# Kernel optimization log

Measured on AMD Instinct MI355X. Metric: run time of the kernel, lower is better.

The kernel has to match this reference:

```python
import jax, jax.numpy as jnp
import numpy as np

SDIM, VDIM, HID, DEPTH = 128, 3, 64, 4
N, E = 50000, 800000
CUTOFF = 5.0


def setup_inputs() -> dict:
    key = jax.random.key(0)
    ks = jax.random.split(key, 16)
    s = jax.random.normal(ks[0], (N, SDIM), jnp.float32)
    v = jax.random.normal(ks[1], (N, 3, VDIM), jnp.float32)
    edge_index = jax.random.randint(ks[2], (2, E), 0, N, dtype=jnp.int32).astype(jnp.int64)
    d = jax.random.uniform(ks[3], (E,), jnp.float32) * CUTOFF
    r = jax.random.normal(ks[4], (E, 3), jnp.float32)
    r = r / jnp.linalg.norm(r, axis=-1, keepdims=True)
    batch = jnp.zeros((N,), jnp.int64)

    def w(k, shape):
        return jax.random.normal(k, shape, jnp.float32) / jnp.sqrt(jnp.float32(shape[-2]))

    return {
        's': s, 'v': v, 'edge_index': edge_index, 'd': d, 'r': r, 'batch': batch,
        'We1': w(ks[5], (DEPTH, 2 * SDIM + 1, HID)), 'be1': jnp.zeros((DEPTH, HID), jnp.float32),
        'We2': w(ks[6], (DEPTH, HID, HID)), 'be2': jnp.zeros((DEPTH, HID), jnp.float32),
        'Wn1': w(ks[7], (DEPTH, SDIM + HID, HID)), 'bn1': jnp.zeros((DEPTH, HID), jnp.float32),
        'Wn2': w(ks[8], (DEPTH, HID, SDIM)), 'bn2': jnp.zeros((DEPTH, SDIM), jnp.float32),
        'Wv': w(ks[9], (DEPTH, HID, 2 * VDIM)), 'bv': jnp.zeros((DEPTH, 2 * VDIM), jnp.float32),
    }


def _egcl(s, v, src, dst, d, r, C, deg, We1, be1, We2, be2, Wn1, bn1, Wn2, bn2, Wv, bv):
    n = s.shape[0]
    # edge message MLP on gathered endpoint features + distance
    x = jnp.concatenate([s[dst], s[src], d[:, None]], axis=-1)   # [E, 2*SDIM+1]
    h = jax.nn.silu(x @ We1 + be1)
    h = jax.nn.silu(h @ We2 + be2)
    h = h * C[:, None]                                            # cutoff envelope
    # scalar update
    agg_s = jax.ops.segment_sum(h, dst, num_segments=n)           # [N, HID]
    u = jax.nn.silu(jnp.concatenate([s, agg_s], axis=-1) @ Wn1 + bn1)
    s = s + (u @ Wn2 + bn2)
    # equivariant vector update: gated neighbor vectors + gated edge directions
    gates = h @ Wv + bv                                           # [E, 2*VDIM]
    g1, g2 = gates[:, :VDIM], gates[:, VDIM:]
    mv = v[src] * g1[:, None, :] + r[:, :, None] * g2[:, None, :] # [E, 3, VDIM]
    agg_v = jax.ops.segment_sum(mv, dst, num_segments=n) / deg[:, None, None]  # mean aggr
    v = v + agg_v
    return s, v


def reference(s, v, edge_index, d, r, batch, We1, be1, We2, be2, Wn1, bn1, Wn2, bn2, Wv, bv):
    src, dst = edge_index[0], edge_index[1]
    C = 0.5 * (jnp.cos(jnp.pi * d / CUTOFF) + 1.0) * (d < CUTOFF).astype(d.dtype)
    deg = jax.ops.segment_sum(jnp.ones_like(d), dst, num_segments=s.shape[0])
    deg = jnp.maximum(deg, 1.0)
    for i in range(DEPTH):
        s, v = _egcl(s, v, src, dst, d, r, C, deg,
                     We1[i], be1[i], We2[i], be2[i],
                     Wn1[i], bn1[i], Wn2[i], bn2[i], Wv[i], bv[i])
    return (s, v)
```

## Files before the change

kernel.cpp:

```cpp
#include <hip/hip_runtime.h>
#include <math.h>

#define SDIM 128
#define HID 64
#define DEPTH 4
#define CUTOFF_F 5.0f
#define CHUNK 4096

typedef __attribute__((ext_vector_type(8))) short bf16x8;
typedef __attribute__((ext_vector_type(4))) float f32x4;
typedef float4 __attribute__((aligned(4))) float4_u;

__device__ __forceinline__ float silu_f(float x) {
    float e = __expf(-x);
    return x * __builtin_amdgcn_rcpf(1.0f + e);
}

__device__ __forceinline__ unsigned short f2bf(float x) {
    __bf16 b = (__bf16)x;
    return __builtin_bit_cast(unsigned short, b);
}
__device__ __forceinline__ unsigned int f2bf2(float a, float b) {
    return (unsigned int)f2bf(a) | ((unsigned int)f2bf(b) << 16);
}
__device__ __forceinline__ float bf2f(unsigned short u) {
    return __uint_as_float(((unsigned int)u) << 16);
}

struct f8 { float v[8]; };
__device__ __forceinline__ f8 load8(const float* p) {
    f8 r;
    float4 a = *(const float4*)p;
    float4 b = *(const float4*)(p + 4);
    r.v[0]=a.x; r.v[1]=a.y; r.v[2]=a.z; r.v[3]=a.w;
    r.v[4]=b.x; r.v[5]=b.y; r.v[6]=b.z; r.v[7]=b.w;
    return r;
}
__device__ __forceinline__ bf16x8 pack8(const float* h) {
    bf16x8 o;
#pragma unroll
    for (int j = 0; j < 8; ++j) o[j] = (short)f2bf(h[j]);
    return o;
}
__device__ __forceinline__ void unpack8(bf16x8 b, float* o) {
#pragma unroll
    for (int j = 0; j < 8; ++j)
        o[j] = __uint_as_float(((unsigned int)(unsigned short)b[j]) << 16);
}

__global__ void detect_idx_kernel(const void* ei, int N, int* flag) {
    int lane = threadIdx.x;
    const long long* p64 = (const long long*)ei;
    long long v = p64[lane];
    bool ok = (v >= 0 && v < (long long)N);
    unsigned long long m = __ballot(ok);
    if (lane == 0) *flag = (m == ~0ull) ? 1 : 0;
}

__global__ void decode_idx_kernel(const void* ei, int E, int N, const int* flag,
                                  int* __restrict__ srcw, int* __restrict__ dstw,
                                  int* __restrict__ deg_i) {
    int i = blockIdx.x * blockDim.x + threadIdx.x;
    if (i >= 2 * E) return;
    int v;
    if (*flag) v = (int)((const long long*)ei)[i];
    else       v = ((const int*)ei)[i];
    v = min(max(v, 0), N - 1);
    if (i < E) {
        srcw[i] = v;
    } else {
        dstw[i - E] = v;
        atomicAdd(&deg_i[v], 1);
    }
}

__global__ __launch_bounds__(256) void scan1_kernel(const int* __restrict__ deg_i,
                                                    int* __restrict__ part, int N) {
    __shared__ int wsum[4];
    int b = blockIdx.x, t = threadIdx.x;
    int base = b * CHUNK;
    int sum = 0;
    for (int i = t; i < CHUNK; i += 256) {
        int idx = base + i;
        sum += (idx < N) ? deg_i[idx] : 0;
    }
#pragma unroll
    for (int off = 32; off; off >>= 1) sum += __shfl_down(sum, off, 64);
    if ((t & 63) == 0) wsum[t >> 6] = sum;
    __syncthreads();
    if (t == 0) part[b] = wsum[0] + wsum[1] + wsum[2] + wsum[3];
}

__global__ void scan2_kernel(int* __restrict__ part, int* __restrict__ row_start,
                             int B1, int N) {
    int t = threadIdx.x;
    int v = (t < B1) ? part[t] : 0;
    int incl = v;
#pragma unroll
    for (int off = 1; off < 64; off <<= 1) {
        int x = __shfl_up(incl, off, 64);
        if (t >= off) incl += x;
    }
    if (t < B1) part[t] = incl - v;
    if (t == 63) row_start[N] = incl;
}

__global__ __launch_bounds__(256) void scan3_kernel(const int* __restrict__ deg_i,
                                                    const int* __restrict__ part,
                                                    int* __restrict__ row_start, int N) {
    __shared__ int wsum[4];
    __shared__ int carry_s;
    int b = blockIdx.x, t = threadIdx.x;
    int lane = t & 63, w = t >> 6;
    if (t == 0) carry_s = part[b];
    __syncthreads();
    int base0 = b * CHUNK;
    for (int base = base0; base < base0 + CHUNK; base += 256) {
        int i = base + t;
        int v = (i < N) ? deg_i[i] : 0;
        int incl = v;
#pragma unroll
        for (int off = 1; off < 64; off <<= 1) {
            int x = __shfl_up(incl, off, 64);
            if (lane >= off) incl += x;
        }
        if (lane == 63) wsum[w] = incl;
        __syncthreads();
        int wpre = 0;
#pragma unroll
        for (int k = 0; k < 4; ++k) if (k < w) wpre += wsum[k];
        int total = wsum[0] + wsum[1] + wsum[2] + wsum[3];
        int carry = carry_s;
        if (i < N) row_start[i] = carry + wpre + incl - v;
        __syncthreads();
        if (t == 0) carry_s = carry + total;
        __syncthreads();
    }
}

__global__ void scatter_kernel(const int* __restrict__ srcw, const int* __restrict__ dstw,
                               const float* __restrict__ dvec, const float* __restrict__ rvec,
                               const int* __restrict__ row_start, int* __restrict__ cursor,
                               float* __restrict__ rec, int E) {
    int e = blockIdx.x * blockDim.x + threadIdx.x;
    if (e >= E) return;
    int dd = dstw[e];
    int ofs = atomicAdd(&cursor[dd], 1);
    int pos = row_start[dd] + ofs;
    float dv = dvec[e];
    float c = 0.5f * (cosf(3.14159265358979323846f * dv * (1.0f / CUTOFF_F)) + 1.0f);
    c = (dv < CUTOFF_F) ? c : 0.0f;
    float4 r0 = make_float4(__int_as_float(srcw[e]), __int_as_float(dd), dv, c);
    float4 r1 = make_float4(rvec[(size_t)e * 3 + 0], rvec[(size_t)e * 3 + 1],
                            rvec[(size_t)e * 3 + 2], 0.0f);
    *(float4*)(rec + (size_t)pos * 8)     = r0;
    *(float4*)(rec + (size_t)pos * 8 + 4) = r1;
}

__global__ __launch_bounds__(256) void wprep_kernel(
    const float* __restrict__ We1, const float* __restrict__ We2,
    const float* __restrict__ Wv,  const float* __restrict__ Wn1,
    const float* __restrict__ Wn2,
    unsigned short* __restrict__ We1t, unsigned short* __restrict__ We2t,
    unsigned short* __restrict__ Wvt,  unsigned short* __restrict__ Wn1t,
    unsigned short* __restrict__ Wn2t) {
    int l = blockIdx.x, t = threadIdx.x;
    const float* W2 = We2 + (size_t)l * HID * HID;
    unsigned short* T2 = We2t + (size_t)l * HID * HID;
    for (int idx = t; idx < HID * HID; idx += 256) {
        int n = idx >> 6, k = idx & 63;
        T2[n * 64 + k] = f2bf(W2[k * HID + n]);
    }
    const float* Wvl = Wv + (size_t)l * HID * 6;
    unsigned short* Tv = Wvt + (size_t)l * 16 * 64;
    for (int idx = t; idx < 16 * 64; idx += 256) {
        int n = idx >> 6, k = idx & 63;
        Tv[idx] = (n < 6) ? f2bf(Wvl[k * 6 + n]) : (unsigned short)0;
    }
    const float* W1 = We1 + (size_t)l * 257 * 64;
    unsigned short* T1 = We1t + (size_t)l * 128 * 128;
    for (int idx = t; idx < 128 * 128; idx += 256) {
        int n = idx >> 7, k = idx & 127;
        float w = (n < 64) ? W1[(size_t)k * 64 + n] : W1[(size_t)(k + 128) * 64 + (n - 64)];
        T1[n * 128 + k] = f2bf(w);
    }
    const float* Wn1l = Wn1 + (size_t)l * 192 * 64;
    unsigned short* Tn1 = Wn1t + (size_t)l * 64 * 192;
    for (int idx = t; idx < 64 * 192; idx += 256) {
        int n = idx / 192, k = idx - n * 192;
        Tn1[idx] = f2bf(Wn1l[(size_t)k * 64 + n]);
    }
    const float* Wn2l = Wn2 + (size_t)l * 64 * 128;
    unsigned short* Tn2 = Wn2t + (size_t)l * 128 * 64;
    for (int idx = t; idx < 128 * 64; idx += 256) {
        int n = idx >> 6, k = idx & 63;
        Tn2[idx] = f2bf(Wn2l[(size_t)k * 128 + n]);
    }
}

__global__ __launch_bounds__(256) void node_pre_kernel(
    const float* __restrict__ s, const unsigned short* __restrict__ We1t,
    const float* __restrict__ be1,
    unsigned short* __restrict__ Pa, unsigned short* __restrict__ Pb, int N)
{
    __shared__ unsigned short sa[64 * 136];
    int t = threadIdx.x;
    int n0 = blockIdx.x * 64;
    for (int idx = t; idx < 64 * 32; idx += 256) {
        int rn = idx >> 5, c4 = (idx & 31) << 2;
        int n = n0 + rn;
        float4 val = make_float4(0.f, 0.f, 0.f, 0.f);
        if (n < N) val = *(const float4*)(s + (size_t)n * SDIM + c4);
        *(uint2*)(sa + rn * 136 + c4) = make_uint2(f2bf2(val.x, val.y), f2bf2(val.z, val.w));
    }
    __syncthreads();
    int lane = t & 63, w = t >> 6;
    int lm = lane & 15, lq = lane >> 4;
    int m0 = w * 16, rm = m0 + lm;

    bf16x8 af[4];
#pragma unroll
    for (int kc = 0; kc < 4; ++kc)
        af[kc] = *(const bf16x8*)(sa + rm * 136 + kc * 32 + lq * 8);

#pragma unroll
    for (int ct = 0; ct < 8; ++ct) {
        int col = ct * 16 + lm;
        f32x4 acc = {0.f, 0.f, 0.f, 0.f};
#pragma unroll
        for (int kc = 0; kc < 4; ++kc) {
            bf16x8 b = *(const bf16x8*)(We1t + (size_t)col * 128 + kc * 32 + lq * 8);
            acc = __builtin_amdgcn_mfma_f32_16x16x32_bf16(af[kc], b, acc, 0, 0, 0);
        }
        float bias = (ct < 4) ? be1[col] : 0.0f;
#pragma unroll
        for (int g = 0; g < 4; ++g) {
            int n = n0 + m0 + lq * 4 + g;
            if (n < N) {
                if (ct < 4) Pa[(size_t)n * HID + col]        = f2bf(acc[g] + bias);
                else        Pb[(size_t)n * HID + (col - 64)] = f2bf(acc[g]);
            }
        }
    }
}

__global__ __launch_bounds__(256) void edge_kernel(
    const float* __restrict__ rec,
    const unsigned short* __restrict__ Pa, const unsigned short* __restrict__ Pb,
    const float* __restrict__ wd,
    const unsigned short* __restrict__ We2t, const float* __restrict__ be2,
    const unsigned short* __restrict__ Wvt, const float* __restrict__ bv,
    const float* __restrict__ v,
    float* __restrict__ agg_s, float* __restrict__ agg_v, int E)
{
    __shared__ unsigned short hb[64 * 72];
    __shared__ float gl[64 * 8];
    __shared__ float vb[64 * 12];
    __shared__ float recb[64 * 8];
    int t = threadIdx.x;
    int e0 = blockIdx.x * 64;

    if (e0 + 64 <= E) {
        float2 rv = *(const float2*)(rec + (size_t)e0 * 8 + 2 * t);
        *(float2*)(recb + 2 * t) = rv;
    } else {
        int r = t >> 2, c = (t & 3) * 2;
        int e = e0 + r;
        int ec = (e < E) ? e : (E - 1);
        float a  = rec[(size_t)ec * 8 + c];
        float b2 = rec[(size_t)ec * 8 + c + 1];
        if (e >= E && c == 2) b2 = 0.0f;
        recb[2 * t]     = a;
        recb[2 * t + 1] = b2;
    }
    __syncthreads();

    int lane = t & 63;
    int w    = t >> 6;
    int lm = lane & 15, lq = lane >> 4;
    int m0 = w * 16;
    int rm = m0 + lm;
    int ka = lq * 8;
    int kb = 32 + lq * 8;

    {
        int r = t >> 2, p = t & 3;
        const float* vr = v + (size_t)__float_as_int(recb[r * 8]) * 9;
        if (p < 2) {
            float4_u a = *(const float4_u*)(vr + p * 4);
            vb[r * 12 + p * 4 + 0] = a.x;
            vb[r * 12 + p * 4 + 1] = a.y;
            vb[r * 12 + p * 4 + 2] = a.z;
            vb[r * 12 + p * 4 + 3] = a.w;
        } else if (p == 2) {
            vb[r * 12 + 8] = vr[8];
        }
    }
    bf16x8 wv0 = *(const bf16x8*)(Wvt + (size_t)lm * 64 + ka);
    bf16x8 wv1 = *(const bf16x8*)(Wvt + (size_t)lm * 64 + kb);

    bf16x8 afr0, afr1;
    {
        int srcr = __float_as_int(recb[rm * 8 + 0]);
        int dstr = __float_as_int(recb[rm * 8 + 1]);
        float dv = recb[rm * 8 + 2];
        const unsigned short* pa = Pa + (size_t)dstr * HID;
        const unsigned short* pb = Pb + (size_t)srcr * HID;
        bf16x8 ba0 = *(const bf16x8*)(pa + ka);
        bf16x8 bb0 = *(const bf16x8*)(pb + ka);
        bf16x8 ba1 = *(const bf16x8*)(pa + kb);
        bf16x8 bb1 = *(const bf16x8*)(pb + kb);
        f8 xw = load8(wd + ka), yw = load8(wd + kb);
        float fa[8], fb[8], h1[8];
        unpack8(ba0, fa); unpack8(bb0, fb);
#pragma unroll
        for (int j = 0; j < 8; ++j) h1[j] = silu_f(fa[j] + fb[j] + dv * xw.v[j]);
        afr0 = pack8(h1);
        unpack8(ba1, fa); unpack8(bb1, fb);
#pragma unroll
        for (int j = 0; j < 8; ++j) h1[j] = silu_f(fa[j] + fb[j] + dv * yw.v[j]);
        afr1 = pack8(h1);
    }

    float cc[4];
#pragma unroll
    for (int g = 0; g < 4; ++g) cc[g] = recb[(m0 + lq * 4 + g) * 8 + 3];
#pragma unroll
    for (int t4 = 0; t4 < 4; ++t4) {
        int col = t4 * 16 + lm;
        bf16x8 b0 = *(const bf16x8*)(We2t + (size_t)col * 64 + ka);
        bf16x8 b1 = *(const bf16x8*)(We2t + (size_t)col * 64 + kb);
        f32x4 a = {0.f, 0.f, 0.f, 0.f};
        a = __builtin_amdgcn_mfma_f32_16x16x32_bf16(afr0, b0, a, 0, 0, 0);
        a = __builtin_amdgcn_mfma_f32_16x16x32_bf16(afr1, b1, a, 0, 0, 0);
        float bias = be2[col];
#pragma unroll
        for (int g = 0; g < 4; ++g) {
            int er = m0 + lq * 4 + g;
            hb[er * 72 + col] = f2bf(silu_f(a[g] + bias) * cc[g]);
        }
    }
    __syncthreads();

    {
        bf16x8 hb0 = *(const bf16x8*)(hb + rm * 72 + ka);
        bf16x8 hb1 = *(const bf16x8*)(hb + rm * 72 + kb);
        f32x4 ga = {0.f, 0.f, 0.f, 0.f};
        ga = __builtin_amdgcn_mfma_f32_16x16x32_bf16(wv0, hb0, ga, 0, 0, 0);
        ga = __builtin_amdgcn_mfma_f32_16x16x32_bf16(wv1, hb1, ga, 0, 0, 0);
        int er2 = m0 + lm;
        if (lq == 0) {
            float4_u bb = *(const float4_u*)bv;
            *(float4*)(gl + er2 * 8) =
                make_float4(ga[0] + bb.x, ga[1] + bb.y, ga[2] + bb.z, ga[3] + bb.w);
        } else if (lq == 1) {
            gl[er2 * 8 + 4] = ga[0] + bv[4];
            gl[er2 * 8 + 5] = ga[1] + bv[5];
        }
    }

    {
        int c = t & 63, seg = t >> 6;
        int r0s = seg * 16;
        float acc = 0.f;
        int cur = __float_as_int(recb[r0s * 8 + 1]);
#pragma unroll 4
        for (int r = r0s; r < r0s + 16; ++r) {
            int dr = __float_as_int(recb[r * 8 + 1]);
            if (dr != cur) {
                atomicAdd(&agg_s[(size_t)cur * HID + c], acc);
                acc = 0.f; cur = dr;
            }
            acc += bf2f(hb[r * 72 + c]);
        }
        atomicAdd(&agg_s[(size_t)cur * HID + c], acc);
    }
    __syncthreads();

    if (t < 144) {
        int seg = t / 9;
        int c = t - seg * 9;
        int i = c / 3, j = c - i * 3;
        int r0v = seg * 4;
        float acc = 0.f;
        int cur = __float_as_int(recb[r0v * 8 + 1]);
#pragma unroll
        for (int r = 0; r < 4; ++r) {
            int rr = r0v + r;
            int dr = __float_as_int(recb[rr * 8 + 1]);
            if (dr != cur) {
                atomicAdd(&agg_v[(size_t)cur * 9 + c], acc);
                acc = 0.f; cur = dr;
            }
            if (e0 + rr < E) {
                acc += vb[rr * 12 + c] * gl[rr * 8 + j]
                     + recb[rr * 8 + 4 + i] * gl[rr * 8 + 3 + j];
            }
        }
        atomicAdd(&agg_v[(size_t)cur * 9 + c], acc);
    }
}

__global__ __launch_bounds__(256) void node_fused_kernel(
    float* __restrict__ s, float* __restrict__ vout,
    float* __restrict__ agg_s, float* __restrict__ agg_v,
    const int* __restrict__ row_start,
    const unsigned short* __restrict__ Wn1t, const float* __restrict__ bn1,
    const unsigned short* __restrict__ Wn2t, const float* __restrict__ bn2,
    const unsigned short* __restrict__ We1tn, const float* __restrict__ be1n,
    unsigned short* __restrict__ Pa, unsigned short* __restrict__ Pb,
    int N, int do_pre)
{
    __shared__ unsigned short xa[64 * 200];
    __shared__ unsigned short ub[64 * 72];
    int t = threadIdx.x;
    int n0 = blockIdx.x * 64;
    for (int idx = t; idx < 64 * 32; idx += 256) {
        int rn = idx >> 5, c4 = (idx & 31) << 2;
        int n = n0 + rn;
        float4 val = make_float4(0.f, 0.f, 0.f, 0.f);
        if (n < N) val = *(const float4*)(s + (size_t)n * SDIM + c4);
        *(uint2*)(xa + rn * 200 + c4) = make_uint2(f2bf2(val.x, val.y), f2bf2(val.z, val.w));
    }
    for (int idx = t; idx < 64 * 16; idx += 256) {
        int rn = idx >> 4, c4 = (idx & 15) << 2;
        int n = n0 + rn;
        float4 val = make_float4(0.f, 0.f, 0.f, 0.f);
        if (n < N) {
            float* ap = agg_s + (size_t)n * HID + c4;
            val = *(const float4*)ap;
            *(float4*)ap = make_float4(0.f, 0.f, 0.f, 0.f);
        }
        *(uint2*)(xa + rn * 200 + 128 + c4) = make_uint2(f2bf2(val.x, val.y), f2bf2(val.z, val.w));
    }
    __syncthreads();

    int lane = t & 63, w = t >> 6;
    int lm = lane & 15, lq = lane >> 4;
    int m0 = w * 16, rm = m0 + lm;

    bf16x8 af[6];
#pragma unroll
    for (int kc = 0; kc < 6; ++kc)
        af[kc] = *(const bf16x8*)(xa + rm * 200 + kc * 32 + lq * 8);

#pragma unroll
    for (int ct = 0; ct < 4; ++ct) {
        int col = ct * 16 + lm;
        f32x4 acc = {0.f, 0.f, 0.f, 0.f};
#pragma unroll
        for (int kc = 0; kc < 6; ++kc) {
            bf16x8 b = *(const bf16x8*)(Wn1t + (size_t)col * 192 + kc * 32 + lq * 8);
            acc = __builtin_amdgcn_mfma_f32_16x16x32_bf16(af[kc], b, acc, 0, 0, 0);
        }
        float bias = bn1[col];
#pragma unroll
        for (int g = 0; g < 4; ++g) {
            int er = m0 + lq * 4 + g;
            ub[er * 72 + col] = f2bf(silu_f(acc[g] + bias));
        }
    }
    __syncthreads();

    unsigned short* sa = xa;
    bf16x8 uf[2];
#pragma unroll
    for (int kc = 0; kc < 2; ++kc)
        uf[kc] = *(const bf16x8*)(ub + rm * 72 + kc * 32 + lq * 8);

#pragma unroll
    for (int ct = 0; ct < 8; ++ct) {
        int col = ct * 16 + lm;
        f32x4 acc = {0.f, 0.f, 0.f, 0.f};
#pragma unroll
        for (int kc = 0; kc < 2; ++kc) {
            bf16x8 b = *(const bf16x8*)(Wn2t + (size_t)col * 64 + kc * 32 + lq * 8);
            acc = __builtin_amdgcn_mfma_f32_16x16x32_bf16(uf[kc], b, acc, 0, 0, 0);
        }
        float bias = bn2[col];
#pragma unroll
        for (int g = 0; g < 4; ++g) {
            int er = m0 + lq * 4 + g;
            int n = n0 + er;
            if (n < N) {
                float* sp = s + (size_t)n * SDIM + col;
                float sv = *sp + acc[g] + bias;
                *sp = sv;
                sa[er * 136 + col] = f2bf(sv);
            } else {
                sa[er * 136 + col] = 0;
            }
        }
    }
    __syncthreads();

    if (do_pre) {
        bf16x8 pf[4];
#pragma unroll
        for (int kc = 0; kc < 4; ++kc)
            pf[kc] = *(const bf16x8*)(sa + rm * 136 + kc * 32 + lq * 8);

#pragma unroll
        for (int ct = 0; ct < 8; ++ct) {
            int col = ct * 16 + lm;
            f32x4 acc = {0.f, 0.f, 0.f, 0.f};
#pragma unroll
            for (int kc = 0; kc < 4; ++kc) {
                bf16x8 b = *(const bf16x8*)(We1tn + (size_t)col * 128 + kc * 32 + lq * 8);
                acc = __builtin_amdgcn_mfma_f32_16x16x32_bf16(pf[kc], b, acc, 0, 0, 0);
            }
            float bias = (ct < 4) ? be1n[col] : 0.0f;
#pragma unroll
            for (int g = 0; g < 4; ++g) {
                int n = n0 + m0 + lq * 4 + g;
                if (n < N) {
                    if (ct < 4) Pa[(size_t)n * HID + col]        = f2bf(acc[g] + bias);
                    else        Pb[(size_t)n * HID + (col - 64)] = f2bf(acc[g]);
                }
            }
        }
    }

    for (int idx = t; idx < 64 * 9; idx += 256) {
        int rn = idx / 9, c = idx - rn * 9;
        int n2 = n0 + rn;
        if (n2 < N) {
            float av = agg_v[(size_t)n2 * 9 + c];
            agg_v[(size_t)n2 * 9 + c] = 0.f;
            float dg = fmaxf((float)(row_start[n2 + 1] - row_start[n2]), 1.0f);
            vout[(size_t)n2 * 9 + c] += av / dg;
        }
    }
}

extern "C" void kernel_launch(void* const* d_in, const int* in_sizes, int n_in,
                              void* d_out, int out_size, void* d_ws, size_t ws_size,
                              hipStream_t stream)
{
    const float* s_in  = (const float*)d_in[0];
    const float* v_in  = (const float*)d_in[1];
    const void*  ei    = d_in[2];
    const float* d_vec = (const float*)d_in[3];
    const float* r_vec = (const float*)d_in[4];
    const float* We1 = (const float*)d_in[6];
    const float* be1 = (const float*)d_in[7];
    const float* We2 = (const float*)d_in[8];
    const float* be2 = (const float*)d_in[9];
    const float* Wn1 = (const float*)d_in[10];
    const float* bn1 = (const float*)d_in[11];
    const float* Wn2 = (const float*)d_in[12];
    const float* bn2 = (const float*)d_in[13];
    const float* Wv  = (const float*)d_in[14];
    const float* bv  = (const float*)d_in[15];

    int N = in_sizes[0] / SDIM;
    int E = in_sizes[3];

    float* out_s = (float*)d_out;
    float* out_v = out_s + (size_t)N * SDIM;

    char* wp = (char*)d_ws;
    auto alloc = [&wp](size_t bytes) -> char* {
        char* p = wp;
        wp += (bytes + 31) & ~(size_t)31;
        return p;
    };
    float* rec       = (float*)alloc((size_t)E * 8 * 4);
    unsigned short* Pa = (unsigned short*)alloc((size_t)N * HID * 2);
    unsigned short* Pb = (unsigned short*)alloc((size_t)N * HID * 2);
    float* agg_s     = (float*)alloc((size_t)N * HID * 4);
    float* agg_v     = (float*)alloc((size_t)N * 9 * 4);
    int*   deg_i     = (int*)alloc((size_t)N * 4);
    int*   cursor    = (int*)alloc((size_t)N * 4);
    int*   row_start = (int*)alloc((size_t)(N + 1) * 4);
    int*   part      = (int*)alloc(64 * 4);
    int*   flag      = (int*)alloc(16);
    int*   srcw      = (int*)alloc((size_t)E * 4);
    int*   dstw      = (int*)alloc((size_t)E * 4);
    unsigned short* We2t = (unsigned short*)alloc((size_t)DEPTH * HID * HID * 2);
    unsigned short* Wvt  = (unsigned short*)alloc((size_t)DEPTH * 16 * 64 * 2);
    unsigned short* We1t = (unsigned short*)alloc((size_t)DEPTH * 128 * 128 * 2);
    unsigned short* Wn1t = (unsigned short*)alloc((size_t)DEPTH * 64 * 192 * 2);
    unsigned short* Wn2t = (unsigned short*)alloc((size_t)DEPTH * 128 * 64 * 2);

    hipMemcpyAsync(out_s, s_in, (size_t)N * SDIM * sizeof(float),
                   hipMemcpyDeviceToDevice, stream);
    hipMemcpyAsync(out_v, v_in, (size_t)N * 9 * sizeof(float),
                   hipMemcpyDeviceToDevice, stream);

    detect_idx_kernel<<<1, 64, 0, stream>>>(ei, N, flag);
    hipMemsetAsync(deg_i, 0, (size_t)N * 2 * sizeof(int), stream);
    hipMemsetAsync(agg_s, 0, (size_t)N * (HID + 9) * sizeof(float), stream);
    decode_idx_kernel<<<(2 * E + 255) / 256, 256, 0, stream>>>(ei, E, N, flag,
                                                               srcw, dstw, deg_i);
    int B1 = (N + CHUNK - 1) / CHUNK;
    scan1_kernel<<<B1, 256, 0, stream>>>(deg_i, part, N);
    scan2_kernel<<<1, 64, 0, stream>>>(part, row_start, B1, N);
    scan3_kernel<<<B1, 256, 0, stream>>>(deg_i, part, row_start, N);
    scatter_kernel<<<(E + 255) / 256, 256, 0, stream>>>(srcw, dstw, d_vec, r_vec,
                                                        row_start, cursor, rec, E);
    wprep_kernel<<<DEPTH, 256, 0, stream>>>(We1, We2, Wv, Wn1, Wn2,
                                            We1t, We2t, Wvt, Wn1t, Wn2t);

    int nb_n = (N + 63) / 64;
    int nb_e = (E + 63) / 64;
    node_pre_kernel<<<nb_n, 256, 0, stream>>>(out_s, We1t, be1, Pa, Pb, N);
    for (int l = 0; l < DEPTH; ++l) {
        int ln = (l + 1 < DEPTH) ? (l + 1) : 0;
        const float* We1_l = We1 + (size_t)l * 257 * 64;
        const float* be2_l = be2 + (size_t)l * 64;
        const float* bn1_l = bn1 + (size_t)l * 64;
        const float* bn2_l = bn2 + (size_t)l * 128;
        const float* bv_l  = bv  + (size_t)l * 6;
        const float* be1_n = be1 + (size_t)ln * 64;
        const unsigned short* We2t_l = We2t + (size_t)l * HID * HID;
        const unsigned short* Wvt_l  = Wvt  + (size_t)l * 16 * 64;
        const unsigned short* Wn1t_l = Wn1t + (size_t)l * 64 * 192;
        const unsigned short* Wn2t_l = Wn2t + (size_t)l * 128 * 64;
        const unsigned short* We1t_n = We1t + (size_t)ln * 128 * 128;

        edge_kernel<<<nb_e, 256, 0, stream>>>(rec, Pa, Pb,
                                              We1_l + 256 * 64,
                                              We2t_l, be2_l, Wvt_l, bv_l,
                                              out_v, agg_s, agg_v, E);
        node_fused_kernel<<<nb_n, 256, 0, stream>>>(out_s, out_v, agg_s, agg_v,
                                                    row_start,
                                                    Wn1t_l, bn1_l, Wn2t_l, bn2_l,
                                                    We1t_n, be1_n, Pa, Pb,
                                                    N, (l + 1 < DEPTH) ? 1 : 0);
    }
}
```

Baseline: 823.1 us.

## Make edge and node kernels wave-local, replacing block barriers with wave barriers

Each wave now owns its 16-row slice of shared memory in the edge, node-pre and node-update kernels, so block-wide __syncthreads are replaced by wave barriers. In the edge kernel the per-edge record is loaded straight into registers with one float4 per row, and the endpoint gathers are issued right away instead of first staging the whole record in LDS. Only dst, C and r are kept in shared memory for the scatter phase. This removes block synchronization stalls and a staging round-trip, at the cost of some redundant record loads across lanes and reliance on wave barriers for correct LDS ordering.

```diff
diff --git a/kernel.cpp b/kernel.cpp
--- a/kernel.cpp
+++ b/kernel.cpp
@@ -203,25 +203,26 @@
     const float* __restrict__ be1,
     unsigned short* __restrict__ Pa, unsigned short* __restrict__ Pb, int N)
 {
-    __shared__ unsigned short sa[64 * 136];
+    __shared__ unsigned short sa[4][16 * 136];
     int t = threadIdx.x;
+    int lane = t & 63, w = t >> 6;
     int n0 = blockIdx.x * 64;
-    for (int idx = t; idx < 64 * 32; idx += 256) {
-        int rn = idx >> 5, c4 = (idx & 31) << 2;
-        int n = n0 + rn;
+    int m0 = w * 16;
+    unsigned short* sw = sa[w];
+    for (int idx = lane; idx < 512; idx += 64) {
+        int rl = idx >> 5, c4 = (idx & 31) << 2;
+        int n = n0 + m0 + rl;
         float4 val = make_float4(0.f, 0.f, 0.f, 0.f);
         if (n < N) val = *(const float4*)(s + (size_t)n * SDIM + c4);
-        *(uint2*)(sa + rn * 136 + c4) = make_uint2(f2bf2(val.x, val.y), f2bf2(val.z, val.w));
-    }
-    __syncthreads();
-    int lane = t & 63, w = t >> 6;
+        *(uint2*)(sw + rl * 136 + c4) = make_uint2(f2bf2(val.x, val.y), f2bf2(val.z, val.w));
+    }
+    __builtin_amdgcn_wave_barrier();
     int lm = lane & 15, lq = lane >> 4;
-    int m0 = w * 16, rm = m0 + lm;
 
     bf16x8 af[4];
 #pragma unroll
     for (int kc = 0; kc < 4; ++kc)
-        af[kc] = *(const bf16x8*)(sa + rm * 136 + kc * 32 + lq * 8);
+        af[kc] = *(const bf16x8*)(sw + lm * 136 + kc * 32 + lq * 8);
 
 #pragma unroll
     for (int ct = 0; ct < 8; ++ct) {
@@ -254,46 +255,46 @@
     float* __restrict__ agg_s, float* __restrict__ agg_v, int E)
 {
     __shared__ unsigned short hb[64 * 72];
-    __shared__ float gl[64 * 8];
-    __shared__ float vb[64 * 12];
-    __shared__ float recb[64 * 8];
+    __shared__ float  gl[64 * 8];
+    __shared__ float  vb[64 * 12];
+    __shared__ int    m_dst[64];
+    __shared__ float  m_C[64];
+    __shared__ float4 m_r4[64];
     int t = threadIdx.x;
     int e0 = blockIdx.x * 64;
-
-    if (e0 + 64 <= E) {
-        float2 rv = *(const float2*)(rec + (size_t)e0 * 8 + 2 * t);
-        *(float2*)(recb + 2 * t) = rv;
-    } else {
-        int r = t >> 2, c = (t & 3) * 2;
-        int e = e0 + r;
-        int ec = (e < E) ? e : (E - 1);
-        float a  = rec[(size_t)ec * 8 + c];
-        float b2 = rec[(size_t)ec * 8 + c + 1];
-        if (e >= E && c == 2) b2 = 0.0f;
-        recb[2 * t]     = a;
-        recb[2 * t + 1] = b2;
-    }
-    __syncthreads();
-
-    int lane = t & 63;
-    int w    = t >> 6;
+    int lane = t & 63, w = t >> 6;
     int lm = lane & 15, lq = lane >> 4;
-    int m0 = w * 16;
-    int rm = m0 + lm;
-    int ka = lq * 8;
-    int kb = 32 + lq * 8;
-
+    int m0 = w * 16, rm = m0 + lm;
+    int ka = lq * 8, kb = 32 + lq * 8;
+
+    int e  = e0 + rm;
+    int ec = min(e, E - 1);
+    float4 r0 = *(const float4*)(rec + (size_t)ec * 8);
+    int srcr = __float_as_int(r0.x);
+    int dstr = __float_as_int(r0.y);
+    float dv = r0.z;
+    float Cr = (e < E) ? r0.w : 0.0f;
+
+    const unsigned short* pa = Pa + (size_t)dstr * HID;
+    const unsigned short* pb = Pb + (size_t)srcr * HID;
+    bf16x8 ba0 = *(const bf16x8*)(pa + ka);
+    bf16x8 bb0 = *(const bf16x8*)(pb + ka);
+    bf16x8 ba1 = *(const bf16x8*)(pa + kb);
+    bf16x8 bb1 = *(const bf16x8*)(pb + kb);
+    f8 xw = load8(wd + ka), yw = load8(wd + kb);
+
+    if (lq == 0) {
+        m_dst[rm] = dstr;
+        m_C[rm]   = Cr;
+        m_r4[rm]  = *(const float4*)(rec + (size_t)ec * 8 + 4);
+    }
     {
-        int r = t >> 2, p = t & 3;
-        const float* vr = v + (size_t)__float_as_int(recb[r * 8]) * 9;
-        if (p < 2) {
-            float4_u a = *(const float4_u*)(vr + p * 4);
-            vb[r * 12 + p * 4 + 0] = a.x;
-            vb[r * 12 + p * 4 + 1] = a.y;
-            vb[r * 12 + p * 4 + 2] = a.z;
-            vb[r * 12 + p * 4 + 3] = a.w;
-        } else if (p == 2) {
-            vb[r * 12 + 8] = vr[8];
+        const float* vr = v + (size_t)srcr * 9;
+        if (lq < 2) {
+            float4_u a = *(const float4_u*)(vr + lq * 4);
+            *(float4*)(vb + rm * 12 + lq * 4) = make_float4(a.x, a.y, a.z, a.w);
+        } else if (lq == 2) {
+            vb[rm * 12 + 8] = vr[8];
         }
     }
     bf16x8 wv0 = *(const bf16x8*)(Wvt + (size_t)lm * 64 + ka);
@@ -301,16 +302,6 @@
 
     bf16x8 afr0, afr1;
     {
-        int srcr = __float_as_int(recb[rm * 8 + 0]);
-        int dstr = __float_as_int(recb[rm * 8 + 1]);
-        float dv = recb[rm * 8 + 2];
-        const unsigned short* pa = Pa + (size_t)dstr * HID;
-        const unsigned short* pb = Pb + (size_t)srcr * HID;
-        bf16x8 ba0 = *(const bf16x8*)(pa + ka);
-        bf16x8 bb0 = *(const bf16x8*)(pb + ka);
-        bf16x8 ba1 = *(const bf16x8*)(pa + kb);
-        bf16x8 bb1 = *(const bf16x8*)(pb + kb);
-        f8 xw = load8(wd + ka), yw = load8(wd + kb);
         float fa[8], fb[8], h1[8];
         unpack8(ba0, fa); unpack8(bb0, fb);
 #pragma unroll
@@ -322,9 +313,10 @@
         afr1 = pack8(h1);
     }
 
+    __builtin_amdgcn_wave_barrier();
     float cc[4];
 #pragma unroll
-    for (int g = 0; g < 4; ++g) cc[g] = recb[(m0 + lq * 4 + g) * 8 + 3];
+    for (int g = 0; g < 4; ++g) cc[g] = m_C[m0 + lq * 4 + g];
 #pragma unroll
     for (int t4 = 0; t4 < 4; ++t4) {
         int col = t4 * 16 + lm;
@@ -340,7 +332,7 @@
             hb[er * 72 + col] = f2bf(silu_f(a[g] + bias) * cc[g]);
         }
     }
-    __syncthreads();
+    __builtin_amdgcn_wave_barrier();
 
     {
         bf16x8 hb0 = *(const bf16x8*)(hb + rm * 72 + ka);
@@ -360,13 +352,12 @@
     }
 
     {
-        int c = t & 63, seg = t >> 6;
-        int r0s = seg * 16;
+        int c = lane;
         float acc = 0.f;
-        int cur = __float_as_int(recb[r0s * 8 + 1]);
+        int cur = m_dst[m0];
 #pragma unroll 4
-        for (int r = r0s; r < r0s + 16; ++r) {
-            int dr = __float_as_int(recb[r * 8 + 1]);
+        for (int r = m0; r < m0 + 16; ++r) {
+            int dr = m_dst[r];
             if (dr != cur) {
                 atomicAdd(&agg_s[(size_t)cur * HID + c], acc);
                 acc = 0.f; cur = dr;
@@ -375,26 +366,27 @@
         }
         atomicAdd(&agg_s[(size_t)cur * HID + c], acc);
     }
-    __syncthreads();
-
-    if (t < 144) {
-        int seg = t / 9;
-        int c = t - seg * 9;
+    __builtin_amdgcn_wave_barrier();
+
+    if (lane < 36) {
+        int seg = lane / 9;
+        int c = lane - seg * 9;
         int i = c / 3, j = c - i * 3;
-        int r0v = seg * 4;
+        int r0v = m0 + seg * 4;
+        const float* mrf = (const float*)m_r4;
         float acc = 0.f;
-        int cur = __float_as_int(recb[r0v * 8 + 1]);
+        int cur = m_dst[r0v];
 #pragma unroll
         for (int r = 0; r < 4; ++r) {
             int rr = r0v + r;
-            int dr = __float_as_int(recb[rr * 8 + 1]);
+            int dr = m_dst[rr];
             if (dr != cur) {
                 atomicAdd(&agg_v[(size_t)cur * 9 + c], acc);
                 acc = 0.f; cur = dr;
             }
             if (e0 + rr < E) {
                 acc += vb[rr * 12 + c] * gl[rr * 8 + j]
-                     + recb[rr * 8 + 4 + i] * gl[rr * 8 + 3 + j];
+                     + mrf[rr * 4 + i] * gl[rr * 8 + 3 + j];
             }
         }
         atomicAdd(&agg_v[(size_t)cur * 9 + c], acc);
@@ -411,38 +403,40 @@
     unsigned short* __restrict__ Pa, unsigned short* __restrict__ Pb,
     int N, int do_pre)
 {
-    __shared__ unsigned short xa[64 * 200];
+    __shared__ unsigned short xa[4][16 * 200];
     __shared__ unsigned short ub[64 * 72];
     int t = threadIdx.x;
+    int lane = t & 63, w = t >> 6;
     int n0 = blockIdx.x * 64;
-    for (int idx = t; idx < 64 * 32; idx += 256) {
-        int rn = idx >> 5, c4 = (idx & 31) << 2;
-        int n = n0 + rn;
+    int m0 = w * 16;
+    unsigned short* xw = xa[w];
+
+    for (int idx = lane; idx < 512; idx += 64) {
+        int rl = idx >> 5, c4 = (idx & 31) << 2;
+        int n = n0 + m0 + rl;
         float4 val = make_float4(0.f, 0.f, 0.f, 0.f);
         if (n < N) val = *(const float4*)(s + (size_t)n * SDIM + c4);
-        *(uint2*)(xa + rn * 200 + c4) = make_uint2(f2bf2(val.x, val.y), f2bf2(val.z, val.w));
-    }
-    for (int idx = t; idx < 64 * 16; idx += 256) {
-        int rn = idx >> 4, c4 = (idx & 15) << 2;
-        int n = n0 + rn;
+        *(uint2*)(xw + rl * 200 + c4) = make_uint2(f2bf2(val.x, val.y), f2bf2(val.z, val.w));
+    }
+    for (int idx = lane; idx < 256; idx += 64) {
+        int rl = idx >> 4, c4 = (idx & 15) << 2;
+        int n = n0 + m0 + rl;
         float4 val = make_float4(0.f, 0.f, 0.f, 0.f);
         if (n < N) {
             float* ap = agg_s + (size_t)n * HID + c4;
             val = *(const float4*)ap;
             *(float4*)ap = make_float4(0.f, 0.f, 0.f, 0.f);
         }
-        *(uint2*)(xa + rn * 200 + 128 + c4) = make_uint2(f2bf2(val.x, val.y), f2bf2(val.z, val.w));
-    }
-    __syncthreads();
-
-    int lane = t & 63, w = t >> 6;
+        *(uint2*)(xw + rl * 200 + 128 + c4) = make_uint2(f2bf2(val.x, val.y), f2bf2(val.z, val.w));
+    }
+    __builtin_amdgcn_wave_barrier();
+
     int lm = lane & 15, lq = lane >> 4;
-    int m0 = w * 16, rm = m0 + lm;
 
     bf16x8 af[6];
 #pragma unroll
     for (int kc = 0; kc < 6; ++kc)
-        af[kc] = *(const bf16x8*)(xa + rm * 200 + kc * 32 + lq * 8);
+        af[kc] = *(const bf16x8*)(xw + lm * 200 + kc * 32 + lq * 8);
 
 #pragma unroll
     for (int ct = 0; ct < 4; ++ct) {
@@ -460,13 +454,13 @@
             ub[er * 72 + col] = f2bf(silu_f(acc[g] + bias));
         }
     }
-    __syncthreads();
-
-    unsigned short* sa = xa;
+    __builtin_amdgcn_wave_barrier();
+
+    unsigned short* sa = xw;
     bf16x8 uf[2];
 #pragma unroll
     for (int kc = 0; kc < 2; ++kc)
-        uf[kc] = *(const bf16x8*)(ub + rm * 72 + kc * 32 + lq * 8);
+        uf[kc] = *(const bf16x8*)(ub + (m0 + lm) * 72 + kc * 32 + lq * 8);
 
 #pragma unroll
     for (int ct = 0; ct < 8; ++ct) {
@@ -480,25 +474,25 @@
         float bias = bn2[col];
 #pragma unroll
         for (int g = 0; g < 4; ++g) {
-            int er = m0 + lq * 4 + g;
-            int n = n0 + er;
+            int erl = lq * 4 + g;
+            int n = n0 + m0 + erl;
             if (n < N) {
                 float* sp = s + (size_t)n * SDIM + col;
                 float sv = *sp + acc[g] + bias;
                 *sp = sv;
-                sa[er * 136 + col] = f2bf(sv);
+                sa[erl * 136 + col] = f2bf(sv);
             } else {
-                sa[er * 136 + col] = 0;
+                sa[erl * 136 + col] = 0;
             }
         }
     }
-    __syncthreads();
+    __builtin_amdgcn_wave_barrier();
 
     if (do_pre) {
         bf16x8 pf[4];
 #pragma unroll
         for (int kc = 0; kc < 4; ++kc)
-            pf[kc] = *(const bf16x8*)(sa + rm * 136 + kc * 32 + lq * 8);
+            pf[kc] = *(const bf16x8*)(sa + lm * 136 + kc * 32 + lq * 8);
 
 #pragma unroll
         for (int ct = 0; ct < 8; ++ct) {
@@ -521,9 +515,9 @@
         }
     }
 
-    for (int idx = t; idx < 64 * 9; idx += 256) {
-        int rn = idx / 9, c = idx - rn * 9;
-        int n2 = n0 + rn;
+    for (int idx = lane; idx < 144; idx += 64) {
+        int rl = idx / 9, c = idx - rl * 9;
+        int n2 = n0 + m0 + rl;
         if (n2 < N) {
             float av = agg_v[(size_t)n2 * 9 + c];
             agg_v[(size_t)n2 * 9 + c] = 0.f;
```

Measured after the change: 815.3 us. Within noise of the previous version (-1.0%).
